# Performance work log

Hardware: AMD Instinct MI355X
Metric: run time of the kernel (lower is better)

## Reference

```python
import jax, jax.numpy as jnp
import numpy as np

IN_FEATURES = 512
ACTION_DIM = 32
TRIL_DIM = ACTION_DIM * (ACTION_DIM + 1) // 2  # 528
BATCH = 65536
# Row-major lower-triangular indices; matches torch boolean-mask assignment order.
_ROWS, _COLS = np.tril_indices(ACTION_DIM)


def setup_inputs() -> dict:
    key = jax.random.key(0)
    k1, k2, k3, k4, k5 = jax.random.split(key, 5)
    logits = jax.random.normal(k1, (BATCH, IN_FEATURES), dtype=jnp.float32)
    best_action = jax.random.normal(k2, (BATCH, ACTION_DIM), dtype=jnp.float32)
    actions = jax.random.normal(k3, (BATCH, ACTION_DIM), dtype=jnp.float32)
    W = jax.random.normal(k4, (TRIL_DIM, IN_FEATURES), dtype=jnp.float32) * 0.02
    b = jax.random.normal(k5, (TRIL_DIM,), dtype=jnp.float32) * 0.02
    return {"logits": logits, "best_action": best_action, "actions": actions, "W": W, "b": b}


def reference(logits, best_action, actions, W, b):
    # Linear: [B, in_features] -> [B, tril_dim]
    flat_trils = logits @ W.T + b
    B = logits.shape[0]
    n = ACTION_DIM
    # Scatter flat vector into lower-triangular slots (row-major order).
    mats = jnp.zeros((B, n, n), dtype=flat_trils.dtype).at[:, _ROWS, _COLS].set(flat_trils)
    diag = jnp.eye(n, dtype=flat_trils.dtype)
    # Square the diagonal entries, keep off-diagonal entries as-is.
    tril = mats * mats * diag + (1.0 - diag) * mats
    action_diff = actions - best_action  # [B, n]
    vec = jnp.einsum('bij,bj->bi', tril, action_diff)  # [B, n]
    advantage = -0.5 * jnp.sum(vec * vec, axis=-1, keepdims=True)  # [B, 1]
    return advantage
```

## Files before the change

### kernel.cpp

```cpp
#include <hip/hip_runtime.h>
#include <hip/hip_bf16.h>


typedef __attribute__((ext_vector_type(8))) __bf16 bf16x8;
typedef __attribute__((ext_vector_type(4))) float f32x4;

#define AS1 __attribute__((address_space(1)))
#define AS3 __attribute__((address_space(3)))

__device__ __forceinline__ unsigned short f2b(float x) {
  unsigned u = __builtin_bit_cast(unsigned, x);
  u += 0x7fffu + ((u >> 16) & 1u);
  return (unsigned short)(u >> 16);
}
__device__ __forceinline__ float b2f(unsigned short h) {
  unsigned u = ((unsigned)h) << 16;
  return __builtin_bit_cast(float, u);
}

#define NFRAG 34
#define WTILE_BYTES 69632
#define A_OFF 69632
#define SMEM_BYTES (69632 + 8192)

__global__ void prep_wp(const float* __restrict__ W, unsigned short* __restrict__ WP) {
  int t = blockIdx.x * 256 + threadIdx.x;
  int lane = t & 63;
  int u = t >> 6;
  int ksl = u & 1;
  int v = u >> 1;
  int nf = v % NFRAG;
  int kstep = v / NFRAG;
  int n = nf * 16 + (lane & 15);
  int k0 = kstep * 64 + ksl * 32 + (lane >> 4) * 8;
  unsigned short h[8];
  if (n < 528) {
    const float* src = W + (size_t)n * 512 + k0;
#pragma unroll
    for (int j = 0; j < 8; ++j) h[j] = f2b(src[j]);
  } else {
#pragma unroll
    for (int j = 0; j < 8; ++j) h[j] = 0;
  }
  uint4 p;
  p.x = (unsigned)h[0] | ((unsigned)h[1] << 16);
  p.y = (unsigned)h[2] | ((unsigned)h[3] << 16);
  p.z = (unsigned)h[4] | ((unsigned)h[5] << 16);
  p.w = (unsigned)h[6] | ((unsigned)h[7] << 16);
  *(uint4*)(WP + (size_t)t * 8) = p;
}

__global__ void __launch_bounds__(256, 2)
adv_kernel(const float* __restrict__ logits,
           const float* __restrict__ best,
           const float* __restrict__ actions,
           const float* __restrict__ bvec,
           const unsigned short* __restrict__ WP,
           float* __restrict__ out) {
  extern __shared__ char smem[];
  const int tid = threadIdx.x;
  const int l   = tid & 63;
  const int wid = tid >> 6;
  const int lr  = l & 15;
  const int lg  = l >> 4;
  const int brow = blockIdx.x * 64;
  const int start = wid * 8 + (wid > 0 ? 1 : 0);

  f32x4 acc[4][9];
  {
    f32x4 zero = {0.f, 0.f, 0.f, 0.f};
#pragma unroll
    for (int m = 0; m < 4; ++m)
#pragma unroll
      for (int n = 0; n < 9; ++n) acc[m][n] = zero;
  }

  const int ar = tid >> 2;
  const int cq = (tid & 3) << 4;

  for (int ks = 0; ks < 8; ++ks) {
    const char* wsrc = (const char*)WP + (size_t)ks * WTILE_BYTES;
#pragma unroll
    for (int q = 0; q < 17; ++q) {
      int off = ((q * 4 + wid) * 64) * 16;
      __builtin_amdgcn_global_load_lds((AS1 unsigned int*)(wsrc + off + l * 16),
                                       (AS3 unsigned int*)(smem + off), 16, 0, 0);
    }
    {
      const float* src = logits + (size_t)(brow + ar) * 512 + ks * 64 + cq;
      float4 x0 = *(const float4*)(src + 0);
      float4 x1 = *(const float4*)(src + 4);
      float4 x2 = *(const float4*)(src + 8);
      float4 x3 = *(const float4*)(src + 12);
      uint4 p0, p1;
      p0.x = f2b(x0.x) | ((unsigned)f2b(x0.y) << 16);
      p0.y = f2b(x0.z) | ((unsigned)f2b(x0.w) << 16);
      p0.z = f2b(x1.x) | ((unsigned)f2b(x1.y) << 16);
      p0.w = f2b(x1.z) | ((unsigned)f2b(x1.w) << 16);
      p1.x = f2b(x2.x) | ((unsigned)f2b(x2.y) << 16);
      p1.y = f2b(x2.z) | ((unsigned)f2b(x2.w) << 16);
      p1.z = f2b(x3.x) | ((unsigned)f2b(x3.y) << 16);
      p1.w = f2b(x3.z) | ((unsigned)f2b(x3.w) << 16);
      char* abase = smem + A_OFF + ar * 128;
      int swz = (ar & 7) << 4;
      int cb  = cq * 2;
      *(uint4*)(abase + ((cb)      ^ swz)) = p0;
      *(uint4*)(abase + ((cb + 16) ^ swz)) = p1;
    }
    __syncthreads();
#pragma unroll
    for (int ksl = 0; ksl < 2; ++ksl) {
      bf16x8 a[4];
#pragma unroll
      for (int m = 0; m < 4; ++m) {
        int arow = m * 16 + lr;
        int bcol = (ksl * 64 + lg * 16) ^ ((arow & 7) << 4);
        a[m] = *(const bf16x8*)(smem + A_OFF + arow * 128 + bcol);
      }
#pragma unroll
      for (int n = 0; n < 9; ++n) {
        int nf = start + n;
        bf16x8 bfr = *(const bf16x8*)(smem + ((nf * 2 + ksl) * 64 + l) * 16);
#pragma unroll
        for (int m = 0; m < 4; ++m)
          acc[m][n] = __builtin_amdgcn_mfma_f32_16x16x32_bf16(a[m], bfr, acc[m][n], 0, 0, 0);
      }
    }
    __syncthreads();
  }

  unsigned short* fl = (unsigned short*)smem;
#pragma unroll
  for (int n = 0; n < 9; ++n) {
    int nf = start + n;
    if (nf >= 33) continue;
    int f = nf * 16 + lr;
    float bb = bvec[f];
#pragma unroll
    for (int m = 0; m < 4; ++m)
#pragma unroll
      for (int r = 0; r < 4; ++r) {
        int row = m * 16 + lg * 4 + r;
        fl[row * 532 + f] = f2b(acc[m][n][r] + bb);
      }
  }
  {
    float* dl = (float*)(smem + A_OFF);
    int row = tid >> 2;
    int j0  = (tid & 3) << 3;
    const float* ap = actions + (size_t)(brow + row) * 32 + j0;
    const float* bp = best    + (size_t)(brow + row) * 32 + j0;
    float4 a0 = *(const float4*)(ap);
    float4 a1 = *(const float4*)(ap + 4);
    float4 b0 = *(const float4*)(bp);
    float4 b1 = *(const float4*)(bp + 4);
    float d[8] = {a0.x - b0.x, a0.y - b0.y, a0.z - b0.z, a0.w - b0.w,
                  a1.x - b1.x, a1.y - b1.y, a1.z - b1.z, a1.w - b1.w};
    int rs = row & 31;
#pragma unroll
    for (int q = 0; q < 8; ++q)
      dl[row * 32 + ((j0 + q) ^ rs)] = d[q];
  }
  __syncthreads();

  {
    int it  = tid & 3;
    int row = tid >> 2;
    const unsigned short* flr = fl + row * 532;
    const float* dlr = (const float*)(smem + A_OFF) + row * 32;
    int rs = row & 31;
    float ssum = 0.f;
#pragma unroll
    for (int ii = 0; ii < 8; ++ii) {
      int i = it + ii * 4;
      int tri = (i * (i + 1)) >> 1;
      float vec = 0.f;
      for (int j = 0; j < i; ++j)
        vec += b2f(flr[tri + j]) * dlr[j ^ rs];
      float dv = b2f(flr[tri + i]);
      vec += dv * dv * dlr[i ^ rs];
      ssum += vec * vec;
    }
    ssum += __shfl_xor(ssum, 1);
    ssum += __shfl_xor(ssum, 2);
    if (it == 0) out[brow + row] = -0.5f * ssum;
  }
}

extern "C" void kernel_launch(void* const* d_in, const int* in_sizes, int n_in,
                              void* d_out, int out_size, void* d_ws, size_t ws_size,
                              hipStream_t stream) {
  const float* logits  = (const float*)d_in[0];
  const float* best    = (const float*)d_in[1];
  const float* actions = (const float*)d_in[2];
  const float* W       = (const float*)d_in[3];
  const float* bvec    = (const float*)d_in[4];
  float* out = (float*)d_out;
  unsigned short* WP = (unsigned short*)d_ws;

  hipLaunchKernelGGL(prep_wp, dim3(136), dim3(256), 0, stream, W, WP);
  int M = in_sizes[0] / 512;
  hipLaunchKernelGGL(adv_kernel, dim3(M / 64), dim3(256), SMEM_BYTES, stream,
                     logits, best, actions, bvec, WP, out);
}
```

Baseline: 76.95 us.

## Double-buffer W and fp32 logits tiles via async LDS loads with 128-row blocks

Restructures the GEMM main loop into a 16-step double-buffered pipeline. Both the packed W tile and the raw fp32 logits tile are staged directly into LDS with global_load_lds, and the logits are converted to bf16 on read from LDS instead of in registers before storing. Blocks grow to 512 threads covering 128 rows, so each W tile is reused by two row groups of waves. This aims to overlap global loads with MFMA work and halve W traffic per row, at the cost of much larger LDS use (about 136 KB per block), which may limit occupancy.

```diff
diff --git a/kernel.cpp b/kernel.cpp
--- a/kernel.cpp
+++ b/kernel.cpp
@@ -19,20 +19,22 @@
 }
 
 #define NFRAG 34
-#define WTILE_BYTES 69632
-#define A_OFF 69632
-#define SMEM_BYTES (69632 + 8192)
+#define WK_BYTES (NFRAG * 1024)
+#define ATILE_BYTES (128 * 32 * 4)
+#define BUF_BYTES (WK_BYTES + ATILE_BYTES)
+#define A_IN_BUF WK_BYTES
+#define FLAT_STRIDE 532
+#define DIFF_OFF (128 * FLAT_STRIDE * 2)
+#define SMEM_BYTES (DIFF_OFF + 128 * 32 * 4)
 
 __global__ void prep_wp(const float* __restrict__ W, unsigned short* __restrict__ WP) {
   int t = blockIdx.x * 256 + threadIdx.x;
   int lane = t & 63;
   int u = t >> 6;
-  int ksl = u & 1;
-  int v = u >> 1;
-  int nf = v % NFRAG;
-  int kstep = v / NFRAG;
+  int nf = u % NFRAG;
+  int k16 = u / NFRAG;
   int n = nf * 16 + (lane & 15);
-  int k0 = kstep * 64 + ksl * 32 + (lane >> 4) * 8;
+  int k0 = k16 * 32 + (lane >> 4) * 8;
   unsigned short h[8];
   if (n < 528) {
     const float* src = W + (size_t)n * 512 + k0;
@@ -50,7 +52,7 @@
   *(uint4*)(WP + (size_t)t * 8) = p;
 }
 
-__global__ void __launch_bounds__(256, 2)
+__global__ void __launch_bounds__(512, 2)
 adv_kernel(const float* __restrict__ logits,
            const float* __restrict__ best,
            const float* __restrict__ actions,
@@ -63,8 +65,10 @@
   const int wid = tid >> 6;
   const int lr  = l & 15;
   const int lg  = l >> 4;
-  const int brow = blockIdx.x * 64;
-  const int start = wid * 8 + (wid > 0 ? 1 : 0);
+  const int wc  = wid & 3;
+  const int wrbase = (wid >> 2) * 64;
+  const int start = wc * 8 + (wc > 0 ? 1 : 0);
+  const int brow = blockIdx.x * 128;
 
   f32x4 acc[4][9];
   {
@@ -75,59 +79,79 @@
       for (int n = 0; n < 9; ++n) acc[m][n] = zero;
   }
 
-  const int ar = tid >> 2;
-  const int cq = (tid & 3) << 4;
-
-  for (int ks = 0; ks < 8; ++ks) {
-    const char* wsrc = (const char*)WP + (size_t)ks * WTILE_BYTES;
-#pragma unroll
-    for (int q = 0; q < 17; ++q) {
-      int off = ((q * 4 + wid) * 64) * 16;
-      __builtin_amdgcn_global_load_lds((AS1 unsigned int*)(wsrc + off + l * 16),
-                                       (AS3 unsigned int*)(smem + off), 16, 0, 0);
-    }
-    {
-      const float* src = logits + (size_t)(brow + ar) * 512 + ks * 64 + cq;
-      float4 x0 = *(const float4*)(src + 0);
-      float4 x1 = *(const float4*)(src + 4);
-      float4 x2 = *(const float4*)(src + 8);
-      float4 x3 = *(const float4*)(src + 12);
-      uint4 p0, p1;
-      p0.x = f2b(x0.x) | ((unsigned)f2b(x0.y) << 16);
-      p0.y = f2b(x0.z) | ((unsigned)f2b(x0.w) << 16);
-      p0.z = f2b(x1.x) | ((unsigned)f2b(x1.y) << 16);
-      p0.w = f2b(x1.z) | ((unsigned)f2b(x1.w) << 16);
-      p1.x = f2b(x2.x) | ((unsigned)f2b(x2.y) << 16);
-      p1.y = f2b(x2.z) | ((unsigned)f2b(x2.w) << 16);
-      p1.z = f2b(x3.x) | ((unsigned)f2b(x3.y) << 16);
-      p1.w = f2b(x3.z) | ((unsigned)f2b(x3.w) << 16);
-      char* abase = smem + A_OFF + ar * 128;
-      int swz = (ar & 7) << 4;
-      int cb  = cq * 2;
-      *(uint4*)(abase + ((cb)      ^ swz)) = p0;
-      *(uint4*)(abase + ((cb + 16) ^ swz)) = p1;
-    }
-    __syncthreads();
-#pragma unroll
-    for (int ksl = 0; ksl < 2; ++ksl) {
-      bf16x8 a[4];
-#pragma unroll
-      for (int m = 0; m < 4; ++m) {
-        int arow = m * 16 + lr;
-        int bcol = (ksl * 64 + lg * 16) ^ ((arow & 7) << 4);
-        a[m] = *(const bf16x8*)(smem + A_OFF + arow * 128 + bcol);
-      }
-#pragma unroll
-      for (int n = 0; n < 9; ++n) {
-        int nf = start + n;
-        bf16x8 bfr = *(const bf16x8*)(smem + ((nf * 2 + ksl) * 64 + l) * 16);
-#pragma unroll
-        for (int m = 0; m < 4; ++m)
-          acc[m][n] = __builtin_amdgcn_mfma_f32_16x16x32_bf16(a[m], bfr, acc[m][n], 0, 0, 0);
-      }
-    }
-    __syncthreads();
-  }
+  int aoff[4][2];
+#pragma unroll
+  for (int m = 0; m < 4; ++m)
+#pragma unroll
+    for (int h = 0; h < 2; ++h)
+      aoff[m][h] = (wrbase + m * 16 + lr) * 128 +
+                   ((lg * 32 + h * 16) ^ ((lr & 7) << 4));
+  int boff[9];
+#pragma unroll
+  for (int n = 0; n < 9; ++n) boff[n] = (start + n) * 1024 + l * 16;
+
+#define STAGE_A(dst, ks)                                                        \
+  {                                                                             \
+    char* dA = (dst) + A_IN_BUF;                                                \
+    _Pragma("unroll")                                                           \
+    for (int p = 0; p < 2; ++p) {                                               \
+      int c = p * 512 + tid;                                                    \
+      int row = c >> 3, hh = c & 7;                                             \
+      const float* g = logits + (size_t)(brow + row) * 512 + (ks) * 32 +        \
+                       ((hh ^ (row & 7)) << 2);                                 \
+      __builtin_amdgcn_global_load_lds((AS1 unsigned int*)g,                    \
+          (AS3 unsigned int*)(dA + (p * 512 + wid * 64) * 16), 16, 0, 0);       \
+    }                                                                           \
+  }
+#define STAGE_W(dst, ks)                                                        \
+  {                                                                             \
+    const char* sW = (const char*)WP + (size_t)(ks) * WK_BYTES;                 \
+    _Pragma("unroll")                                                           \
+    for (int q = 0; q < 4; ++q) {                                               \
+      int off = (q * 8 + wid) * 1024;                                           \
+      __builtin_amdgcn_global_load_lds((AS1 unsigned int*)(sW + off + l * 16),  \
+          (AS3 unsigned int*)((dst) + off), 16, 0, 0);                          \
+    }                                                                           \
+    if (wid < 2) {                                                              \
+      int off = (32 + wid) * 1024;                                              \
+      __builtin_amdgcn_global_load_lds((AS1 unsigned int*)(sW + off + l * 16),  \
+          (AS3 unsigned int*)((dst) + off), 16, 0, 0);                          \
+    }                                                                           \
+  }
+
+  STAGE_A(smem, 0)
+  STAGE_W(smem, 0)
+  __syncthreads();
+
+  for (int t = 0; t < 16; ++t) {
+    char* buf = smem + (t & 1) * BUF_BYTES;
+    if (t < 15) {
+      char* nb = smem + ((t & 1) ^ 1) * BUF_BYTES;
+      STAGE_A(nb, t + 1)
+      STAGE_W(nb, t + 1)
+    }
+    bf16x8 a[4];
+#pragma unroll
+    for (int m = 0; m < 4; ++m) {
+      f32x4 x0 = *(const f32x4*)(buf + A_IN_BUF + aoff[m][0]);
+      f32x4 x1 = *(const f32x4*)(buf + A_IN_BUF + aoff[m][1]);
+      bf16x8 af;
+      af[0] = (__bf16)x0[0]; af[1] = (__bf16)x0[1];
+      af[2] = (__bf16)x0[2]; af[3] = (__bf16)x0[3];
+      af[4] = (__bf16)x1[0]; af[5] = (__bf16)x1[1];
+      af[6] = (__bf16)x1[2]; af[7] = (__bf16)x1[3];
+      a[m] = af;
+    }
+#pragma unroll
+    for (int n = 0; n < 9; ++n) {
+      bf16x8 bfr = *(const bf16x8*)(buf + boff[n]);
+#pragma unroll
+      for (int m = 0; m < 4; ++m)
+        acc[m][n] = __builtin_amdgcn_mfma_f32_16x16x32_bf16(a[m], bfr, acc[m][n], 0, 0, 0);
+    }
+    if (t < 15) __syncthreads();
+  }
+  __syncthreads();
 
   unsigned short* fl = (unsigned short*)smem;
 #pragma unroll
@@ -140,12 +164,12 @@
     for (int m = 0; m < 4; ++m)
 #pragma unroll
       for (int r = 0; r < 4; ++r) {
-        int row = m * 16 + lg * 4 + r;
-        fl[row * 532 + f] = f2b(acc[m][n][r] + bb);
+        int row = wrbase + m * 16 + lg * 4 + r;
+        fl[row * FLAT_STRIDE + f] = f2b(acc[m][n][r] + bb);
       }
   }
   {
-    float* dl = (float*)(smem + A_OFF);
+    float* dl = (float*)(smem + DIFF_OFF);
     int row = tid >> 2;
     int j0  = (tid & 3) << 3;
     const float* ap = actions + (size_t)(brow + row) * 32 + j0;
@@ -166,8 +190,8 @@
   {
     int it  = tid & 3;
     int row = tid >> 2;
-    const unsigned short* flr = fl + row * 532;
-    const float* dlr = (const float*)(smem + A_OFF) + row * 32;
+    const unsigned short* flr = fl + row * FLAT_STRIDE;
+    const float* dlr = (const float*)(smem + DIFF_OFF) + row * 32;
     int rs = row & 31;
     float ssum = 0.f;
 #pragma unroll
@@ -200,6 +224,6 @@
 
   hipLaunchKernelGGL(prep_wp, dim3(136), dim3(256), 0, stream, W, WP);
   int M = in_sizes[0] / 512;
-  hipLaunchKernelGGL(adv_kernel, dim3(M / 64), dim3(256), SMEM_BYTES, stream,
+  hipLaunchKernelGGL(adv_kernel, dim3(M / 128), dim3(512), SMEM_BYTES, stream,
                      logits, best, actions, bvec, WP, out);
 }
```

Measured after the change: 61.82 us. -19.7%, faster.
